# Kernel tuning notes

Measured on AMD Instinct MI355X. Metric: run time of the kernel, lower is better.

## Reference

```python
import jax, jax.numpy as jnp
import numpy as np

N_NODES = 100000
N_EDGES = 3200000


def _gcn_conv(x, W, b, src, dst, dinv, n_nodes):
    """PyG GCNConv: linear -> symmetric-normalized scatter-add over (self-looped) edges -> bias."""
    h = x @ W  # [N, out]
    norm = (dinv[src] * dinv[dst])[:, None]  # [E+N, 1]
    msg = h[src] * norm  # gather + scale
    out = jax.ops.segment_sum(msg, dst, num_segments=n_nodes)  # scatter-add
    return out + b


def setup_inputs() -> dict:
    key = jax.random.key(0)
    ks = jax.random.split(key, 16)
    x = jax.random.normal(ks[0], (N_NODES, 512), dtype=jnp.float32)
    edge_index = jax.random.randint(ks[1], (2, N_EDGES), 0, N_NODES, dtype=jnp.int32)

    def glorot(k, fan_in, fan_out):
        s = jnp.sqrt(6.0 / (fan_in + fan_out))
        return jax.random.uniform(k, (fan_in, fan_out), jnp.float32, -s, s)

    dims = [(512, 64), (64, 8), (8, 4), (4, 2), (4, 2)]
    names = ["1", "2", "3", "mu", "lv"]
    params = {}
    for i, ((fi, fo), nm) in enumerate(zip(dims, names)):
        params[f"W{nm}"] = glorot(ks[2 + i], fi, fo)
        params[f"b{nm}"] = jnp.zeros((fo,), jnp.float32)
    return {"x": x, "edge_index": edge_index, **params}


def reference(x, edge_index, W1, b1, W2, b2, W3, b3, Wmu, bmu, Wlv, blv):
    n = x.shape[0]
    loops = jnp.arange(n, dtype=edge_index.dtype)
    src = jnp.concatenate([edge_index[0], loops])  # add self-loops
    dst = jnp.concatenate([edge_index[1], loops])
    deg = jax.ops.segment_sum(jnp.ones_like(dst, dtype=x.dtype), dst, num_segments=n)
    dinv = jnp.where(deg > 0, jax.lax.rsqrt(jnp.maximum(deg, 1.0)), 0.0)

    h = jax.nn.relu(_gcn_conv(x, W1, b1, src, dst, dinv, n))
    h = jax.nn.relu(_gcn_conv(h, W2, b2, src, dst, dinv, n))
    h = jax.nn.relu(_gcn_conv(h, W3, b3, src, dst, dinv, n))
    mu = _gcn_conv(h, Wmu, bmu, src, dst, dinv, n)
    logvar = _gcn_conv(h, Wlv, blv, src, dst, dinv, n)
    return mu, logvar
```

## Files before the change

kernel.cpp:

```cpp
#include <hip/hip_runtime.h>
#include <hip/hip_fp16.h>
#include <stdint.h>


#define BSHIFT 7
#define BPB 128
#define CAP 5632
#define NBMAX 800
#define CAPB 40

__global__ __launch_bounds__(1024) void k_part(const int* __restrict__ esrc, const int* __restrict__ edst,
                                               int* __restrict__ bcnt, int* __restrict__ pairs,
                                               int E, int NB, int nblocks) {
  __shared__ int bincnt[NBMAX];
  __shared__ int sflushed[NBMAX];
  __shared__ int binbuf[NBMAX * CAPB];
  const int tid = threadIdx.x;
  for (int b = tid; b < NB; b += 1024) { bincnt[b] = 0; sflushed[b] = 0; }
  __syncthreads();
  const int chunk = (E + nblocks - 1) / nblocks;
  const int e0 = blockIdx.x * chunk;
  const int e1 = min(e0 + chunk, E);
  for (int base = e0; base < e1; base += 1024) {
    int e = base + tid;
    if (e < e1) {
      int d = edst[e], s = esrc[e];
      int b = d >> BSHIFT;
      int pos = atomicAdd(&bincnt[b], 1);
      binbuf[b * CAPB + (pos % CAPB)] = (s << BSHIFT) | (d & (BPB - 1));
    }
    __syncthreads();
    if (tid < NB) {
      int c = bincnt[tid], f = sflushed[tid];
      while (c - f >= 16) {
        int p = atomicAdd(&bcnt[tid * 16], 16);
#pragma unroll
        for (int j = 0; j < 16; ++j)
          pairs[(size_t)tid * CAP + p + j] = binbuf[tid * CAPB + ((f + j) % CAPB)];
        f += 16;
      }
      sflushed[tid] = f;
    }
    __syncthreads();
  }
  if (tid < NB) {
    int c = bincnt[tid], f = sflushed[tid];
    int rem = c - f;
    if (rem > 0) {
      int p = atomicAdd(&bcnt[tid * 16], rem);
      for (int j = 0; j < rem; ++j)
        pairs[(size_t)tid * CAP + p + j] = binbuf[tid * CAPB + ((f + j) % CAPB)];
    }
  }
}

__global__ __launch_bounds__(256, 4) void k_gemm1(const float* __restrict__ x, const float* __restrict__ W,
                                                  __half* __restrict__ h1, int n) {
  __shared__ float xs[32 * 128];
  __shared__ float ws[32 * 64];
  const int tid = threadIdx.x;
  const int n0 = blockIdx.x * 128;
  const int tn = tid & 31;
  const int tf = tid >> 5;
  const int lr = tid >> 3;
  const int lc = tid & 7;

  float4 px[4], pw[2];
  auto ldg_tile = [&](int kt) {
#pragma unroll
    for (int i = 0; i < 4; ++i) {
      int r = n0 + lr + i * 32;
      if (r >= n) r = n - 1;
      px[i] = *(const float4*)(x + (size_t)r * 512 + kt + lc * 4);
    }
#pragma unroll
    for (int i = 0; i < 2; ++i) {
      int idx = tid + 256 * i;
      int k = idx >> 4, f4 = idx & 15;
      pw[i] = *(const float4*)(W + (size_t)(kt + k) * 64 + f4 * 4);
    }
  };

  float acc[4][8];
#pragma unroll
  for (int i = 0; i < 4; ++i)
#pragma unroll
    for (int j = 0; j < 8; ++j) acc[i][j] = 0.f;

  ldg_tile(0);
  for (int t = 0; t < 16; ++t) {
    __syncthreads();
    {
      const int sw = 8 * (lc & 3);
#pragma unroll
      for (int i = 0; i < 4; ++i) {
        int r = (lr + i * 32) ^ sw;
        xs[(lc * 4 + 0) * 128 + r] = px[i].x;
        xs[(lc * 4 + 1) * 128 + r] = px[i].y;
        xs[(lc * 4 + 2) * 128 + r] = px[i].z;
        xs[(lc * 4 + 3) * 128 + r] = px[i].w;
      }
#pragma unroll
      for (int i = 0; i < 2; ++i) {
        int idx = tid + 256 * i;
        *(float4*)&ws[(idx >> 4) * 64 + (idx & 15) * 4] = pw[i];
      }
    }
    __syncthreads();
    if (t < 15) ldg_tile((t + 1) * 32);
#pragma unroll 8
    for (int k = 0; k < 32; ++k) {
      float4 xv = *(const float4*)&xs[k * 128 + ((tn * 4) ^ (8 * ((k >> 2) & 3)))];
      float4 w0 = *(const float4*)&ws[k * 64 + tf * 8];
      float4 w1 = *(const float4*)&ws[k * 64 + tf * 8 + 4];
      float xa[4] = {xv.x, xv.y, xv.z, xv.w};
      float wb[8] = {w0.x, w0.y, w0.z, w0.w, w1.x, w1.y, w1.z, w1.w};
#pragma unroll
      for (int i = 0; i < 4; ++i)
#pragma unroll
        for (int j = 0; j < 8; ++j) acc[i][j] = fmaf(xa[i], wb[j], acc[i][j]);
    }
  }
#pragma unroll
  for (int i = 0; i < 4; ++i) {
    int node = n0 + tn * 4 + i;
    if (node < n) {
      union { int4 v; __half h[8]; } u;
#pragma unroll
      for (int j = 0; j < 8; ++j) u.h[j] = __float2half_rn(acc[i][j]);
      *(int4*)(h1 + (size_t)node * 64 + tf * 8) = u.v;
    }
  }
}

__global__ __launch_bounds__(1024) void k_bscan(const int* __restrict__ bcnt, int* __restrict__ bbase,
                                                int* __restrict__ offs, int NB, int n, int E) {
  __shared__ int sc[1024];
  int tid = threadIdx.x;
  int v = (tid < NB) ? bcnt[tid * 16] : 0;
  sc[tid] = v;
  __syncthreads();
  for (int d = 1; d < 1024; d <<= 1) {
    int t = (tid >= d) ? sc[tid - d] : 0;
    __syncthreads();
    if (tid >= d) sc[tid] += t;
    __syncthreads();
  }
  if (tid < NB) bbase[tid] = sc[tid] - v;
  if (tid == 0) offs[n] = E;
}

__global__ __launch_bounds__(1024) void k_p2(const int* __restrict__ pairs, const int* __restrict__ bcnt,
                                             const int* __restrict__ bbase, int* __restrict__ offs,
                                             float* __restrict__ dinv, int* __restrict__ csr, int n) {
  __shared__ int lcnt[BPB];
  __shared__ int scanv[BPB];
  __shared__ int cur[BPB];
  __shared__ int sbuf[CAP];
  const int tid = threadIdx.x;
  const int b = blockIdx.x;
  const int size = bcnt[b * 16];
  const int base = bbase[b];
  const int node0 = b << BSHIFT;
  const int nb = min(BPB, n - node0);

  if (tid < BPB) lcnt[tid] = 0;
  __syncthreads();

  int stash[6];
  int ns = 0;
  for (int i = tid; i < size; i += 1024) {
    int w = pairs[(size_t)b * CAP + i];
    stash[ns++] = w;
    atomicAdd(&lcnt[w & (BPB - 1)], 1);
  }
  __syncthreads();
  if (tid < BPB) scanv[tid] = lcnt[tid];
  __syncthreads();
#pragma unroll
  for (int d = 1; d < BPB; d <<= 1) {
    int t = (tid < BPB && tid >= d) ? scanv[tid - d] : 0;
    __syncthreads();
    if (tid < BPB && tid >= d) scanv[tid] += t;
    __syncthreads();
  }
  if (tid < nb) {
    int excl = scanv[tid] - lcnt[tid];
    offs[node0 + tid] = base + excl;
    cur[tid] = excl;
    dinv[node0 + tid] = rsqrtf((float)(lcnt[tid] + 1));
  }
  __syncthreads();
  for (int i = 0; i < ns; ++i) {
    int w = stash[i];
    int p = atomicAdd(&cur[w & (BPB - 1)], 1);
    sbuf[p] = w >> BSHIFT;
  }
  __syncthreads();
  for (int i = tid; i < size; i += 1024) csr[base + i] = sbuf[i];
}

__global__ __launch_bounds__(256) void k_pull64(const __half* __restrict__ h, const int* __restrict__ offs,
                                                const int* __restrict__ csr, const float* __restrict__ dinv,
                                                const float* __restrict__ b1, const float* __restrict__ W2,
                                                float* __restrict__ h2, int n) {
  __shared__ float sa[4][64];
  __shared__ float w2s[512];
  const int tid = threadIdx.x;
  w2s[tid] = W2[tid];
  w2s[tid + 256] = W2[tid + 256];
  const int lane = tid & 63;
  const int wv = tid >> 6;
  const int node = blockIdx.x * 4 + wv;
  float a1v = 0.f;
  if (node < n) {
    int s0 = offs[node], s1 = offs[node + 1];
    float di = dinv[node];
    float acc = 0.f;
    int e = s0;
    for (; e + 4 <= s1; e += 4) {
      int i0 = csr[e], i1 = csr[e + 1], i2 = csr[e + 2], i3 = csr[e + 3];
      float w0 = dinv[i0], w1 = dinv[i1], w2 = dinv[i2], w3 = dinv[i3];
      float v0 = __half2float(h[(size_t)i0 * 64 + lane]);
      float v1 = __half2float(h[(size_t)i1 * 64 + lane]);
      float v2 = __half2float(h[(size_t)i2 * 64 + lane]);
      float v3 = __half2float(h[(size_t)i3 * 64 + lane]);
      acc = fmaf(w0, v0, acc); acc = fmaf(w1, v1, acc);
      acc = fmaf(w2, v2, acc); acc = fmaf(w3, v3, acc);
    }
    for (; e < s1; ++e) {
      int s = csr[e];
      acc = fmaf(dinv[s], __half2float(h[(size_t)s * 64 + lane]), acc);
    }
    acc = fmaf(di, __half2float(h[(size_t)node * 64 + lane]), acc);
    a1v = fmaxf(fmaf(di, acc, b1[lane]), 0.f);
  }
  sa[wv][lane] = a1v;
  __syncthreads();
  if (tid < 32) {
    int j = tid >> 3, f = tid & 7;
    int nd = blockIdx.x * 4 + j;
    if (nd < n) {
      float s = 0.f;
#pragma unroll
      for (int l = 0; l < 64; ++l) s = fmaf(sa[j][l], w2s[l * 8 + f], s);
      h2[(size_t)nd * 8 + f] = s;
    }
  }
}

__global__ __launch_bounds__(256) void k_pull8(const float* __restrict__ h, const int* __restrict__ offs,
                                               const int* __restrict__ csr, const float* __restrict__ dinv,
                                               const float* __restrict__ b2, const float* __restrict__ W3,
                                               float* __restrict__ h3, int n) {
  __shared__ float sa[4][8];
  __shared__ float w3s[32];
  const int tid = threadIdx.x;
  if (tid < 32) w3s[tid] = W3[tid];
  const int lane = tid & 63;
  const int wv = tid >> 6;
  const int node = blockIdx.x * 4 + wv;
  const int j8 = lane >> 3, f = lane & 7;
  float pacc = 0.f;
  float di = 0.f;
  if (node < n) {
    int s0 = offs[node], s1 = offs[node + 1];
    di = dinv[node];
    for (int e0 = s0; e0 < s1; e0 += 8) {
      int e = e0 + j8;
      if (e < s1) {
        int s = csr[e];
        pacc = fmaf(dinv[s], h[(size_t)s * 8 + f], pacc);
      }
    }
  }
  pacc += __shfl_down(pacc, 32);
  pacc += __shfl_down(pacc, 16);
  pacc += __shfl_down(pacc, 8);
  if (node < n && lane < 8) {
    float v = pacc + di * h[(size_t)node * 8 + f];
    sa[wv][f] = fmaxf(fmaf(di, v, b2[f]), 0.f);
  }
  __syncthreads();
  if (tid < 16) {
    int j = tid >> 2, ff = tid & 3;
    int nd = blockIdx.x * 4 + j;
    if (nd < n) {
      float s = 0.f;
#pragma unroll
      for (int k = 0; k < 8; ++k) s = fmaf(sa[j][k], w3s[k * 4 + ff], s);
      h3[(size_t)nd * 4 + ff] = s;
    }
  }
}

__global__ __launch_bounds__(256) void k_pull4(const float* __restrict__ h, const int* __restrict__ offs,
                                               const int* __restrict__ csr, const float* __restrict__ dinv,
                                               const float* __restrict__ b3, float* __restrict__ out, int n) {
  const int tid = threadIdx.x;
  const int lane = tid & 63;
  const int node = blockIdx.x * 4 + (tid >> 6);
  if (node >= n) return;
  const int j16 = lane >> 2, f = lane & 3;
  int s0 = offs[node], s1 = offs[node + 1];
  float di = dinv[node];
  float pacc = 0.f;
  for (int e0 = s0; e0 < s1; e0 += 16) {
    int e = e0 + j16;
    if (e < s1) {
      int s = csr[e];
      pacc = fmaf(dinv[s], h[(size_t)s * 4 + f], pacc);
    }
  }
  pacc += __shfl_down(pacc, 32);
  pacc += __shfl_down(pacc, 16);
  pacc += __shfl_down(pacc, 8);
  pacc += __shfl_down(pacc, 4);
  if (lane < 4) {
    float v = pacc + di * h[(size_t)node * 4 + f];
    out[(size_t)node * 4 + f] = fmaxf(fmaf(di, v, b3[f]), 0.f);
  }
}

__global__ __launch_bounds__(256) void k_pull4o(const float* __restrict__ a3, const int* __restrict__ offs,
                                                const int* __restrict__ csr, const float* __restrict__ dinv,
                                                const float* __restrict__ Wmu, const float* __restrict__ bmu,
                                                const float* __restrict__ Wlv, const float* __restrict__ blv,
                                                float* __restrict__ outp, int n) {
  __shared__ float sg[4][4];
  const int tid = threadIdx.x;
  const int lane = tid & 63;
  const int wv = tid >> 6;
  const int node = blockIdx.x * 4 + wv;
  const int j16 = lane >> 2, f = lane & 3;
  float pacc = 0.f;
  float di = 0.f;
  if (node < n) {
    int s0 = offs[node], s1 = offs[node + 1];
    di = dinv[node];
    for (int e0 = s0; e0 < s1; e0 += 16) {
      int e = e0 + j16;
      if (e < s1) {
        int s = csr[e];
        pacc = fmaf(dinv[s], a3[(size_t)s * 4 + f], pacc);
      }
    }
  }
  pacc += __shfl_down(pacc, 32);
  pacc += __shfl_down(pacc, 16);
  pacc += __shfl_down(pacc, 8);
  pacc += __shfl_down(pacc, 4);
  if (node < n && lane < 4) {
    float v = pacc + di * a3[(size_t)node * 4 + f];
    sg[wv][f] = di * v;
  }
  __syncthreads();
  if (tid < 16) {
    int j = tid >> 2, c = tid & 3;
    int nd = blockIdx.x * 4 + j;
    if (nd < n) {
      const float* Wp = (c < 2) ? Wmu : Wlv;
      const float* bp = (c < 2) ? bmu : blv;
      int cc = c & 1;
      float s = bp[cc];
#pragma unroll
      for (int k = 0; k < 4; ++k) s = fmaf(sg[j][k], Wp[k * 2 + cc], s);
      size_t base = (c < 2) ? 0 : (size_t)2 * n;
      outp[base + (size_t)nd * 2 + cc] = s;
    }
  }
}

extern "C" void kernel_launch(void* const* d_in, const int* in_sizes, int n_in,
                              void* d_out, int out_size, void* d_ws, size_t ws_size,
                              hipStream_t stream) {
  const float* x = (const float*)d_in[0];
  const int* ei = (const int*)d_in[1];
  const float* W1 = (const float*)d_in[2];
  const float* b1 = (const float*)d_in[3];
  const float* W2 = (const float*)d_in[4];
  const float* b2 = (const float*)d_in[5];
  const float* W3 = (const float*)d_in[6];
  const float* b3 = (const float*)d_in[7];
  const float* Wmu = (const float*)d_in[8];
  const float* bmu = (const float*)d_in[9];
  const float* Wlv = (const float*)d_in[10];
  const float* blv = (const float*)d_in[11];
  float* out = (float*)d_out;

  const int N = in_sizes[0] / 512;
  const int E = in_sizes[1] / 2;
  const int* esrc = ei;
  const int* edst = ei + E;
  const int NB = (N + BPB - 1) >> BSHIFT;

  char* w = (char*)d_ws;
  size_t p = 0;
  auto alloc = [&](size_t bytes) -> void* {
    void* r = w + p;
    p = (p + bytes + 255) & ~(size_t)255;
    return r;
  };
  int* bcnt = (int*)alloc((size_t)NB * 16 * 4);
  int* bbase = (int*)alloc((size_t)NB * 4);
  int* offs = (int*)alloc((size_t)(N + 1) * 4);
  float* dinv = (float*)alloc((size_t)N * 4);
  int* csr = (int*)alloc((size_t)E * 4);
  int* pairs = (int*)alloc((size_t)NB * CAP * 4);
  __half* h1 = (__half*)alloc((size_t)N * 64 * 2);
  float* h2 = (float*)alloc((size_t)N * 8 * 4);
  float* h3 = (float*)alloc((size_t)N * 4 * 4);
  float* a3 = (float*)alloc((size_t)N * 4 * 4);

  hipMemsetAsync(bcnt, 0, (size_t)NB * 16 * 4, stream);

  k_part<<<256, 1024, 0, stream>>>(esrc, edst, bcnt, pairs, E, NB, 256);
  k_gemm1<<<(N + 127) / 128, 256, 0, stream>>>(x, W1, h1, N);
  k_bscan<<<1, 1024, 0, stream>>>(bcnt, bbase, offs, NB, N, E);
  k_p2<<<NB, 1024, 0, stream>>>(pairs, bcnt, bbase, offs, dinv, csr, N);

  k_pull64<<<(N + 3) / 4, 256, 0, stream>>>(h1, offs, csr, dinv, b1, h2 ? W2 : W2, h2, N);
  k_pull8<<<(N + 3) / 4, 256, 0, stream>>>(h2, offs, csr, dinv, b2, W3, h3, N);
  k_pull4<<<(N + 3) / 4, 256, 0, stream>>>(h3, offs, csr, dinv, b3, a3, N);
  k_pull4o<<<(N + 3) / 4, 256, 0, stream>>>(a3, offs, csr, dinv, Wmu, bmu, Wlv, blv, out, N);
}
```

Before: 651.2 us.

## Compute first-layer GEMM with fp16 MFMA instead of fp32 FMA

New measurement: 627.2 us. 3.7% less time.

```diff
diff --git a/kernel.cpp b/kernel.cpp
--- a/kernel.cpp
+++ b/kernel.cpp
@@ -8,6 +8,9 @@
 #define CAP 5632
 #define NBMAX 800
 #define CAPB 40
+
+typedef _Float16 f16x8 __attribute__((ext_vector_type(8)));
+typedef float f32x4 __attribute__((ext_vector_type(4)));
 
 __global__ __launch_bounds__(1024) void k_part(const int* __restrict__ esrc, const int* __restrict__ edst,
                                                int* __restrict__ bcnt, int* __restrict__ pairs,
@@ -54,83 +57,87 @@
   }
 }
 
-__global__ __launch_bounds__(256, 4) void k_gemm1(const float* __restrict__ x, const float* __restrict__ W,
-                                                  __half* __restrict__ h1, int n) {
-  __shared__ float xs[32 * 128];
-  __shared__ float ws[32 * 64];
-  const int tid = threadIdx.x;
-  const int n0 = blockIdx.x * 128;
-  const int tn = tid & 31;
-  const int tf = tid >> 5;
-  const int lr = tid >> 3;
-  const int lc = tid & 7;
-
-  float4 px[4], pw[2];
-  auto ldg_tile = [&](int kt) {
-#pragma unroll
-    for (int i = 0; i < 4; ++i) {
-      int r = n0 + lr + i * 32;
-      if (r >= n) r = n - 1;
-      px[i] = *(const float4*)(x + (size_t)r * 512 + kt + lc * 4);
-    }
-#pragma unroll
-    for (int i = 0; i < 2; ++i) {
-      int idx = tid + 256 * i;
-      int k = idx >> 4, f4 = idx & 15;
-      pw[i] = *(const float4*)(W + (size_t)(kt + k) * 64 + f4 * 4);
-    }
+__global__ __launch_bounds__(256) void k_wprep(const float* __restrict__ W, _Float16* __restrict__ wf) {
+  int idx = blockIdx.x * 256 + threadIdx.x;
+  int l = idx & 63, st = idx >> 6;
+  int t = st & 3, s = st >> 2;
+  int kg = l >> 4, c = l & 15;
+  f16x8 v;
+#pragma unroll
+  for (int j = 0; j < 8; ++j)
+    v[j] = (_Float16)W[(size_t)(s * 32 + kg * 8 + j) * 64 + t * 16 + c];
+  *(f16x8*)(wf + (size_t)idx * 8) = v;
+}
+
+__global__ __launch_bounds__(256) void k_gemm1m(const float* __restrict__ x, const _Float16* __restrict__ wf,
+                                                __half* __restrict__ h1, int n) {
+  const int tid = threadIdx.x;
+  const int lane = tid & 63;
+  const int wv = tid >> 6;
+  const int n0 = blockIdx.x * 128 + wv * 32;
+  const int kg = lane >> 4;
+  const int rr = lane & 15;
+
+  const float* xr0 = x + (size_t)min(n0 + rr, n - 1) * 512 + kg * 8;
+  const float* xr1 = x + (size_t)min(n0 + 16 + rr, n - 1) * 512 + kg * 8;
+  const f16x8* wfp = (const f16x8*)wf + lane;
+
+  float4 abuf[2][2][2];
+  f16x8 wbuf[2][4];
+
+  auto ldA = [&](float4 a[2][2], int t) {
+    const int off = t * 32;
+    a[0][0] = *(const float4*)(xr0 + off);
+    a[0][1] = *(const float4*)(xr0 + off + 4);
+    a[1][0] = *(const float4*)(xr1 + off);
+    a[1][1] = *(const float4*)(xr1 + off + 4);
   };
-
-  float acc[4][8];
-#pragma unroll
-  for (int i = 0; i < 4; ++i)
-#pragma unroll
-    for (int j = 0; j < 8; ++j) acc[i][j] = 0.f;
-
-  ldg_tile(0);
+  auto ldW = [&](f16x8 w[4], int t) {
+#pragma unroll
+    for (int j = 0; j < 4; ++j) w[j] = wfp[(t * 4 + j) * 64];
+  };
+  auto cvt8 = [&](const float4& lo, const float4& hi) -> f16x8 {
+    f16x8 r;
+    r[0] = (_Float16)lo.x; r[1] = (_Float16)lo.y; r[2] = (_Float16)lo.z; r[3] = (_Float16)lo.w;
+    r[4] = (_Float16)hi.x; r[5] = (_Float16)hi.y; r[6] = (_Float16)hi.z; r[7] = (_Float16)hi.w;
+    return r;
+  };
+
+  f32x4 acc[2][4];
+#pragma unroll
+  for (int m = 0; m < 2; ++m)
+#pragma unroll
+    for (int j = 0; j < 4; ++j) acc[m][j] = (f32x4){0.f, 0.f, 0.f, 0.f};
+
+  ldA(abuf[0], 0);
+  ldW(wbuf[0], 0);
+#pragma unroll
   for (int t = 0; t < 16; ++t) {
-    __syncthreads();
-    {
-      const int sw = 8 * (lc & 3);
-#pragma unroll
-      for (int i = 0; i < 4; ++i) {
-        int r = (lr + i * 32) ^ sw;
-        xs[(lc * 4 + 0) * 128 + r] = px[i].x;
-        xs[(lc * 4 + 1) * 128 + r] = px[i].y;
-        xs[(lc * 4 + 2) * 128 + r] = px[i].z;
-        xs[(lc * 4 + 3) * 128 + r] = px[i].w;
+    const int cur = t & 1, nxt = cur ^ 1;
+    if (t + 1 < 16) {
+      ldA(abuf[nxt], t + 1);
+      ldW(wbuf[nxt], t + 1);
+    }
+    f16x8 am0 = cvt8(abuf[cur][0][0], abuf[cur][0][1]);
+    f16x8 am1 = cvt8(abuf[cur][1][0], abuf[cur][1][1]);
+#pragma unroll
+    for (int j = 0; j < 4; ++j) {
+      acc[0][j] = __builtin_amdgcn_mfma_f32_16x16x32_f16(am0, wbuf[cur][j], acc[0][j], 0, 0, 0);
+      acc[1][j] = __builtin_amdgcn_mfma_f32_16x16x32_f16(am1, wbuf[cur][j], acc[1][j], 0, 0, 0);
+    }
+  }
+
+#pragma unroll
+  for (int m = 0; m < 2; ++m)
+#pragma unroll
+    for (int r = 0; r < 4; ++r) {
+      int node = n0 + m * 16 + kg * 4 + r;
+      if (node < n) {
+#pragma unroll
+        for (int j = 0; j < 4; ++j)
+          h1[(size_t)node * 64 + j * 16 + rr] = __float2half_rn(acc[m][j][r]);
       }
-#pragma unroll
-      for (int i = 0; i < 2; ++i) {
-        int idx = tid + 256 * i;
-        *(float4*)&ws[(idx >> 4) * 64 + (idx & 15) * 4] = pw[i];
-      }
-    }
-    __syncthreads();
-    if (t < 15) ldg_tile((t + 1) * 32);
-#pragma unroll 8
-    for (int k = 0; k < 32; ++k) {
-      float4 xv = *(const float4*)&xs[k * 128 + ((tn * 4) ^ (8 * ((k >> 2) & 3)))];
-      float4 w0 = *(const float4*)&ws[k * 64 + tf * 8];
-      float4 w1 = *(const float4*)&ws[k * 64 + tf * 8 + 4];
-      float xa[4] = {xv.x, xv.y, xv.z, xv.w};
-      float wb[8] = {w0.x, w0.y, w0.z, w0.w, w1.x, w1.y, w1.z, w1.w};
-#pragma unroll
-      for (int i = 0; i < 4; ++i)
-#pragma unroll
-        for (int j = 0; j < 8; ++j) acc[i][j] = fmaf(xa[i], wb[j], acc[i][j]);
-    }
-  }
-#pragma unroll
-  for (int i = 0; i < 4; ++i) {
-    int node = n0 + tn * 4 + i;
-    if (node < n) {
-      union { int4 v; __half h[8]; } u;
-#pragma unroll
-      for (int j = 0; j < 8; ++j) u.h[j] = __float2half_rn(acc[i][j]);
-      *(int4*)(h1 + (size_t)node * 64 + tf * 8) = u.v;
-    }
-  }
+    }
 }
 
 __global__ __launch_bounds__(1024) void k_bscan(const int* __restrict__ bcnt, int* __restrict__ bbase,
@@ -411,15 +418,17 @@
   float* h2 = (float*)alloc((size_t)N * 8 * 4);
   float* h3 = (float*)alloc((size_t)N * 4 * 4);
   float* a3 = (float*)alloc((size_t)N * 4 * 4);
+  _Float16* wf = (_Float16*)alloc((size_t)512 * 64 * 2);
 
   hipMemsetAsync(bcnt, 0, (size_t)NB * 16 * 4, stream);
 
+  k_wprep<<<16, 256, 0, stream>>>(W1, wf);
   k_part<<<256, 1024, 0, stream>>>(esrc, edst, bcnt, pairs, E, NB, 256);
-  k_gemm1<<<(N + 127) / 128, 256, 0, stream>>>(x, W1, h1, N);
+  k_gemm1m<<<(N + 127) / 128, 256, 0, stream>>>(x, wf, h1, N);
   k_bscan<<<1, 1024, 0, stream>>>(bcnt, bbase, offs, NB, N, E);
   k_p2<<<NB, 1024, 0, stream>>>(pairs, bcnt, bbase, offs, dinv, csr, N);
 
-  k_pull64<<<(N + 3) / 4, 256, 0, stream>>>(h1, offs, csr, dinv, b1, h2 ? W2 : W2, h2, N);
+  k_pull64<<<(N + 3) / 4, 256, 0, stream>>>(h1, offs, csr, dinv, b1, W2, h2, N);
   k_pull8<<<(N + 3) / 4, 256, 0, stream>>>(h2, offs, csr, dinv, b2, W3, h3, N);
   k_pull4<<<(N + 3) / 4, 256, 0, stream>>>(h3, offs, csr, dinv, b3, a3, N);
   k_pull4o<<<(N + 3) / 4, 256, 0, stream>>>(a3, offs, csr, dinv, Wmu, bmu, Wlv, blv, out, N);
```
